# Kernel optimization log

Hardware: AMD Instinct MI355X
Metric: run time of the kernel (lower is better)

Reference implementation:

```python
import jax, jax.numpy as jnp
import numpy as np

D_MODEL = 1024
N_HEADS = 16
HEAD_DIM = D_MODEL // N_HEADS
MAX_LEN = 2048
BATCH = 2
SEQ = 2048


def setup_inputs() -> dict:
    key = jax.random.key(0)
    ks = jax.random.split(key, 6)
    std = 1.0 / np.sqrt(D_MODEL)
    x = jax.random.normal(ks[0], (BATCH, SEQ, D_MODEL), dtype=jnp.float32)
    Wqkv = jax.random.uniform(ks[1], (D_MODEL, 3 * D_MODEL), minval=-std, maxval=std, dtype=jnp.float32)
    bqkv = jax.random.uniform(ks[2], (3 * D_MODEL,), minval=-std, maxval=std, dtype=jnp.float32)
    Wout = jax.random.uniform(ks[3], (D_MODEL, D_MODEL), minval=-std, maxval=std, dtype=jnp.float32)
    bout = jax.random.uniform(ks[4], (D_MODEL,), minval=-std, maxval=std, dtype=jnp.float32)
    rel_pos_bias = 0.02 * jax.random.normal(ks[5], (2 * MAX_LEN - 1,), dtype=jnp.float32)
    return {"x": x, "Wqkv": Wqkv, "bqkv": bqkv, "Wout": Wout, "bout": bout, "rel_pos_bias": rel_pos_bias}


def reference(x, Wqkv, bqkv, Wout, bout, rel_pos_bias):
    B, S, _ = x.shape
    scale = HEAD_DIM ** -0.5
    qkv = x @ Wqkv + bqkv                       # [B,S,3*dm]
    qkv = qkv.reshape(B, S, 3, N_HEADS, HEAD_DIM)
    qkv = jnp.transpose(qkv, (2, 0, 3, 1, 4))   # [3,B,H,S,D]
    q, k, v = qkv[0], qkv[1], qkv[2]
    scores = jnp.einsum('bhqd,bhkd->bhqk', q, k) * scale
    pos = jnp.arange(S)
    rel = jnp.clip(pos[:, None] - pos[None, :] + (MAX_LEN - 1), 0, 2 * MAX_LEN - 2)
    scores = scores + rel_pos_bias[rel][None, None]  # bias shared over batch & heads
    probs = jax.nn.softmax(scores, axis=-1)
    out = jnp.einsum('bhqk,bhkd->bhqd', probs, v)    # [B,H,S,D]
    out = jnp.transpose(out, (0, 2, 1, 3)).reshape(B, S, D_MODEL)
    return out @ Wout + bout
```

## Files before the change

### kernel.cpp

```cpp
#include <hip/hip_runtime.h>
#include <cmath>

#define B_ 2
#define S_ 2048
#define H_ 16
#define D_ 64
#define DM 1024

typedef unsigned short u16;
using short8 = __attribute__((ext_vector_type(8))) short;
using f32x4  = __attribute__((ext_vector_type(4))) float;
using f32x16 = __attribute__((ext_vector_type(16))) float;
using i32x4  = __attribute__((ext_vector_type(4))) int;
typedef float uf4 __attribute__((ext_vector_type(4), aligned(4)));

__device__ __forceinline__ u16 f32_to_bf16(float f) {
    unsigned int u = __float_as_uint(f);
    u += 0x7fffu + ((u >> 16) & 1u);
    return (u16)(u >> 16);
}

__device__ __forceinline__ float exp2_fast(float x) {
    float r;
    asm("v_exp_f32 %0, %1" : "=v"(r) : "v"(x));
    return r;
}

__device__ __forceinline__ int cvt_pk_bf16(float lo, float hi) {
    int r;
    asm("v_cvt_pk_bf16_f32 %0, %1, %2" : "=v"(r) : "v"(lo), "v"(hi));
    return r;
}

__device__ __forceinline__ void gl_lds16(const void* src, void* dst) {
    __builtin_amdgcn_global_load_lds(
        (const __attribute__((address_space(1))) unsigned int*)src,
        (__attribute__((address_space(3))) unsigned int*)dst, 16, 0, 0);
}

__device__ __forceinline__ f32x16 mfma32(short8 a, short8 b, f32x16 c) {
    return __builtin_amdgcn_mfma_f32_32x32x16_bf16(a, b, c, 0, 0, 0);
}

__global__ __launch_bounds__(256) void relattn_prep(
    const float* __restrict__ x, const float* __restrict__ Wqkv,
    const float* __restrict__ Wout, const float* __restrict__ relb,
    u16* __restrict__ xb, u16* __restrict__ WqkvT, u16* __restrict__ WoutT,
    float* __restrict__ relb2)
{
    __shared__ float T[64][65];
    const int tid = threadIdx.x;
    int blk = blockIdx.x;
    if (blk >= 3072) {
        int i0 = ((blk - 3072) * 256 + tid) * 4;
#pragma unroll
        for (int j = 0; j < 4; ++j)
            if (i0 + j < 2 * 2048 - 1)
                relb2[i0 + j] = relb[i0 + j] * 1.44269504f;
        return;
    }
    if (blk < 2048) {
        size_t base = ((size_t)blk * 256 + tid) * 8;
        float4 v0 = *(const float4*)(x + base);
        float4 v1 = *(const float4*)(x + base + 4);
        ushort4 p0 = make_ushort4(f32_to_bf16(v0.x), f32_to_bf16(v0.y),
                                  f32_to_bf16(v0.z), f32_to_bf16(v0.w));
        ushort4 p1 = make_ushort4(f32_to_bf16(v1.x), f32_to_bf16(v1.y),
                                  f32_to_bf16(v1.z), f32_to_bf16(v1.w));
        *(ushort4*)(xb + base) = p0;
        *(ushort4*)(xb + base + 4) = p1;
        return;
    }
    int id = blk - 2048;
    const float* in; u16* outp; int R, C;
    if (id < 768) { in = Wqkv; outp = WqkvT; R = 1024; C = 3072; }
    else          { id -= 768; in = Wout;  outp = WoutT; R = 1024; C = 1024; }
    const int tpr = C >> 6;
    const int r0 = (id / tpr) << 6, c0 = (id % tpr) << 6;
#pragma unroll
    for (int it = 0; it < 4; ++it) {
        int e = tid + it * 256;
        int row = e >> 4, c4 = (e & 15) << 2;
        float4 v = *(const float4*)(in + (size_t)(r0 + row) * C + c0 + c4);
        T[row][c4 + 0] = v.x; T[row][c4 + 1] = v.y;
        T[row][c4 + 2] = v.z; T[row][c4 + 3] = v.w;
    }
    __syncthreads();
#pragma unroll
    for (int it = 0; it < 4; ++it) {
        int e = tid + it * 256;
        int crow = e >> 4, r4 = (e & 15) << 2;
        ushort4 pk = make_ushort4(f32_to_bf16(T[r4 + 0][crow]), f32_to_bf16(T[r4 + 1][crow]),
                                  f32_to_bf16(T[r4 + 2][crow]), f32_to_bf16(T[r4 + 3][crow]));
        *(ushort4*)(outp + (size_t)(c0 + crow) * R + r0 + r4) = pk;
    }
}

__global__ __launch_bounds__(256) void relattn_gemm_qkv(
    const u16* __restrict__ A, const u16* __restrict__ Bm,
    const float* __restrict__ bias, u16* __restrict__ qk, u16* __restrict__ Vt)
{
    __shared__ alignas(16) unsigned char AsB[16384];
    __shared__ alignas(16) unsigned char BsB[16384];
    const int tid = threadIdx.x;
    const int w = tid >> 6, l = tid & 63, ln = l & 15, hi = l >> 4;
    const int wr = w >> 1, wc = w & 1;
    const int row0 = blockIdx.y * 128, col0 = blockIdx.x * 128;
    const char* Ab = (const char*)A;
    const char* Bb = (const char*)Bm;

    f32x4 acc[4][4] = {};
    for (int step = 0; step < 16; ++step) {
        __syncthreads();
#pragma unroll
        for (int it = 0; it < 4; ++it) {
            int dsto = it * 4096 + w * 1024;
            int o = dsto + l * 16;
            int row = o >> 7;
            int swz = (o & 127) ^ ((row & 7) << 4);
            gl_lds16(Ab + (size_t)(row0 + row) * 2048 + step * 128 + swz, AsB + dsto);
            gl_lds16(Bb + (size_t)(col0 + row) * 2048 + step * 128 + swz, BsB + dsto);
        }
        __syncthreads();
#pragma unroll
        for (int kk = 0; kk < 2; ++kk) {
            short8 a[4], b[4];
            const int kb = hi * 16 + kk * 64;
#pragma unroll
            for (int m = 0; m < 4; ++m) {
                int row = wr * 64 + m * 16 + ln;
                a[m] = *(const short8*)(AsB + row * 128 + (kb ^ ((row & 7) << 4)));
            }
#pragma unroll
            for (int n = 0; n < 4; ++n) {
                int row = wc * 64 + n * 16 + ln;
                b[n] = *(const short8*)(BsB + row * 128 + (kb ^ ((row & 7) << 4)));
            }
#pragma unroll
            for (int m = 0; m < 4; ++m)
#pragma unroll
                for (int n = 0; n < 4; ++n)
                    acc[m][n] = __builtin_amdgcn_mfma_f32_16x16x32_bf16(a[m], b[n], acc[m][n], 0, 0, 0);
        }
    }

    const int t = col0 >> 10;
    const int bb = row0 >> 11;
    if (t < 2) {
#pragma unroll
        for (int n = 0; n < 4; ++n) {
            int c = col0 + wc * 64 + n * 16 + ln;
            int h = (c >> 6) & 15, d = c & 63;
            float bv = bias[c];
            u16* plane = qk + (size_t)((t * B_ + bb) * H_ + h) * S_ * D_;
#pragma unroll
            for (int m = 0; m < 4; ++m)
#pragma unroll
                for (int r = 0; r < 4; ++r) {
                    int s = (row0 + wr * 64 + m * 16 + hi * 4 + r) & (S_ - 1);
                    plane[(size_t)s * D_ + d] = f32_to_bf16(acc[m][n][r] + bv);
                }
        }
    } else {
#pragma unroll
        for (int n = 0; n < 4; ++n) {
            int c = col0 + wc * 64 + n * 16 + ln;
            int h = (c >> 6) & 15, d = c & 63;
            float bv = bias[c];
            u16* vrow = Vt + (size_t)((bb * H_ + h) * D_ + d) * S_;
#pragma unroll
            for (int m = 0; m < 4; ++m) {
                int s = (row0 + wr * 64 + m * 16 + hi * 4) & (S_ - 1);
                ushort4 pk = make_ushort4(f32_to_bf16(acc[m][n][0] + bv),
                                          f32_to_bf16(acc[m][n][1] + bv),
                                          f32_to_bf16(acc[m][n][2] + bv),
                                          f32_to_bf16(acc[m][n][3] + bv));
                *(ushort4*)(vrow + s) = pk;
            }
        }
    }
}

__global__ __launch_bounds__(512, 4) void relattn_attn(
    const u16* __restrict__ qk, const u16* __restrict__ Vt,
    const float* __restrict__ relb2, u16* __restrict__ aout)
{
    __shared__ alignas(16) unsigned char Lds[65536];
    const int tid = threadIdx.x;
    const int w = tid >> 6, l = tid & 63;
    const int wg = w & 3, g = w >> 2;
    const int l31 = l & 31, h2 = l >> 5;
    const int qt = blockIdx.x, bh = blockIdx.y;
    const int bb = bh >> 4;
    const char* qpl = (const char*)(qk + (size_t)bh * (S_ * D_));
    const char* kpl = (const char*)(qk + (size_t)(B_ * H_ + bh) * (S_ * D_));
    const char* vpl = (const char*)(Vt + (size_t)bh * (D_ * S_));
    unsigned char* GB = Lds + g * 32768;

    const int q0 = qt * 128 + wg * 32;
    const int qrow = q0 + l31;
    const int kvbase = g * 1024;

    short8 qf[4];
#pragma unroll
    for (int kd = 0; kd < 4; ++kd)
        qf[kd] = *(const short8*)(qpl + (size_t)qrow * 128 + kd * 32 + h2 * 16);

    f32x16 O0 = {}, O1 = {};
    float lrun = 0.f;

    {
#pragma unroll
        for (int it = 0; it < 2; ++it) {
            int dsto = it * 4096 + wg * 1024;
            int o = dsto + l * 16;
            int row = o >> 7;
            int swz = (o & 127) ^ ((row & 7) << 4);
            gl_lds16(kpl + (size_t)(kvbase + row) * 128 + swz, GB + dsto);
            gl_lds16(vpl + (size_t)row * (S_ * 2) + kvbase * 2 + swz, GB + 8192 + dsto);
        }
    }
    __syncthreads();

    for (int kt = 0; kt < 16; ++kt) {
        const int buf = kt & 1;
        const unsigned char* KB = GB + buf * 16384;
        const unsigned char* VB = KB + 8192;
        const int kv0 = kvbase + kt * 64;

        if (kt < 15) {
#pragma unroll
            for (int it = 0; it < 2; ++it) {
                int dsto = it * 4096 + wg * 1024;
                int o = dsto + l * 16;
                int row = o >> 7;
                int swz = (o & 127) ^ ((row & 7) << 4);
                unsigned char* db = GB + (buf ^ 1) * 16384 + dsto;
                gl_lds16(kpl + (size_t)(kv0 + 64 + row) * 128 + swz, db);
                gl_lds16(vpl + (size_t)row * (S_ * 2) + (kv0 + 64) * 2 + swz, db + 8192);
            }
        }

        const float* bp0 = relb2 + (qrow - kv0 - 4 * h2 + 2047);
        uf4 bv0[4], bv1[4];
#pragma unroll
        for (int rq = 0; rq < 4; ++rq) {
            bv0[rq] = *(const uf4*)(bp0 - 8 * rq - 3);
            bv1[rq] = *(const uf4*)(bp0 - 32 - 8 * rq - 3);
        }

        f32x16 s0 = {}, s1 = {};
#pragma unroll
        for (int kd = 0; kd < 4; ++kd) {
            int kbyte = kd * 32 + h2 * 16;
            int sw = (l31 & 7) << 4;
            short8 k0 = *(const short8*)(KB + l31 * 128 + (kbyte ^ sw));
            short8 k1 = *(const short8*)(KB + (32 + l31) * 128 + (kbyte ^ sw));
            s0 = mfma32(k0, qf[kd], s0);
            s1 = mfma32(k1, qf[kd], s1);
        }

        const float SC2 = 0.125f * 1.44269504f;
#pragma unroll
        for (int rq = 0; rq < 4; ++rq)
#pragma unroll
            for (int j = 0; j < 4; ++j) {
                s0[rq * 4 + j] = exp2_fast(s0[rq * 4 + j] * SC2 + bv0[rq][3 - j]);
                s1[rq * 4 + j] = exp2_fast(s1[rq * 4 + j] * SC2 + bv1[rq][3 - j]);
            }

        float q0s = ((s0[0] + s0[1]) + (s0[2] + s0[3])) + ((s0[4] + s0[5]) + (s0[6] + s0[7]));
        float q1s = ((s0[8] + s0[9]) + (s0[10] + s0[11])) + ((s0[12] + s0[13]) + (s0[14] + s0[15]));
        float q2s = ((s1[0] + s1[1]) + (s1[2] + s1[3])) + ((s1[4] + s1[5]) + (s1[6] + s1[7]));
        float q3s = ((s1[8] + s1[9]) + (s1[10] + s1[11])) + ((s1[12] + s1[13]) + (s1[14] + s1[15]));
        lrun += (q0s + q1s) + (q2s + q3s);

#pragma unroll
        for (int ts = 0; ts < 4; ++ts) {
            float p0, p1, p2, p3, p4, p5, p6, p7;
            if (ts == 0)      { p0=s0[0];  p1=s0[1];  p2=s0[2];  p3=s0[3];  p4=s0[4];  p5=s0[5];  p6=s0[6];  p7=s0[7]; }
            else if (ts == 1) { p0=s0[8];  p1=s0[9];  p2=s0[10]; p3=s0[11]; p4=s0[12]; p5=s0[13]; p6=s0[14]; p7=s0[15]; }
            else if (ts == 2) { p0=s1[0];  p1=s1[1];  p2=s1[2];  p3=s1[3];  p4=s1[4];  p5=s1[5];  p6=s1[6];  p7=s1[7]; }
            else              { p0=s1[8];  p1=s1[9];  p2=s1[10]; p3=s1[11]; p4=s1[12]; p5=s1[13]; p6=s1[14]; p7=s1[15]; }
            int c01 = cvt_pk_bf16(p0, p1), c23 = cvt_pk_bf16(p2, p3);
            int c45 = cvt_pk_bf16(p4, p5), c67 = cvt_pk_bf16(p6, p7);
            int px01 = __shfl_xor(c01, 32), px23 = __shfl_xor(c23, 32);
            int px45 = __shfl_xor(c45, 32), px67 = __shfl_xor(c67, 32);
            i32x4 pw;
            pw[0] = h2 ? px45 : c01;
            pw[1] = h2 ? px67 : c23;
            pw[2] = h2 ? c45 : px01;
            pw[3] = h2 ? c67 : px23;
            short8 pb = __builtin_bit_cast(short8, pw);
            int vbyte = ts * 32 + h2 * 16;
            int sw = (l31 & 7) << 4;
            short8 v0 = *(const short8*)(VB + l31 * 128 + (vbyte ^ sw));
            short8 v1 = *(const short8*)(VB + (32 + l31) * 128 + (vbyte ^ sw));
            O0 = mfma32(v0, pb, O0);
            O1 = mfma32(v1, pb, O1);
        }
        __syncthreads();
    }

    lrun += __shfl_xor(lrun, 32);

    {
        float* PO = (float*)(Lds + wg * 8448);
        float* PL = (float*)(Lds + wg * 8448 + 8192);
        if (g == 1) {
#pragma unroll
            for (int r = 0; r < 16; ++r) {
                PO[l * 32 + r] = O0[r];
                PO[l * 32 + 16 + r] = O1[r];
            }
            PL[l] = lrun;
        }
        __syncthreads();
        if (g == 1) return;
        float inv = 1.0f / (lrun + PL[l]);
        const float* src = PO + l * 32;
        u16* orow = aout + (size_t)(bb * S_ + qrow) * DM + (bh & 15) * 64 + 4 * h2;
#pragma unroll
        for (int gq = 0; gq < 4; ++gq) {
            float o00 = (O0[4*gq+0] + src[4*gq+0]) * inv;
            float o01 = (O0[4*gq+1] + src[4*gq+1]) * inv;
            float o02 = (O0[4*gq+2] + src[4*gq+2]) * inv;
            float o03 = (O0[4*gq+3] + src[4*gq+3]) * inv;
            float o10 = (O1[4*gq+0] + src[16+4*gq+0]) * inv;
            float o11 = (O1[4*gq+1] + src[16+4*gq+1]) * inv;
            float o12 = (O1[4*gq+2] + src[16+4*gq+2]) * inv;
            float o13 = (O1[4*gq+3] + src[16+4*gq+3]) * inv;
            ushort4 w0 = make_ushort4(f32_to_bf16(o00), f32_to_bf16(o01), f32_to_bf16(o02), f32_to_bf16(o03));
            ushort4 w1 = make_ushort4(f32_to_bf16(o10), f32_to_bf16(o11), f32_to_bf16(o12), f32_to_bf16(o13));
            *(ushort4*)(orow + 8 * gq) = w0;
            *(ushort4*)(orow + 32 + 8 * gq) = w1;
        }
    }
}

__global__ __launch_bounds__(256) void relattn_gemm_out(
    const u16* __restrict__ A, const u16* __restrict__ Bm,
    const float* __restrict__ bias, float* __restrict__ out)
{
    __shared__ alignas(16) unsigned char AsB[16384];
    __shared__ alignas(16) unsigned char BsB[16384];
    const int tid = threadIdx.x;
    const int w = tid >> 6, l = tid & 63, ln = l & 15, hi = l >> 4;
    const int wr = w >> 1, wc = w & 1;
    const int row0 = blockIdx.y * 128, col0 = blockIdx.x * 128;
    const char* Ab = (const char*)A;
    const char* Bb = (const char*)Bm;

    f32x4 acc[4][4] = {};
    for (int step = 0; step < 16; ++step) {
        __syncthreads();
#pragma unroll
        for (int it = 0; it < 4; ++it) {
            int dsto = it * 4096 + w * 1024;
            int o = dsto + l * 16;
            int row = o >> 7;
            int swz = (o & 127) ^ ((row & 7) << 4);
            gl_lds16(Ab + (size_t)(row0 + row) * 2048 + step * 128 + swz, AsB + dsto);
            gl_lds16(Bb + (size_t)(col0 + row) * 2048 + step * 128 + swz, BsB + dsto);
        }
        __syncthreads();
#pragma unroll
        for (int kk = 0; kk < 2; ++kk) {
            short8 a[4], b[4];
            const int kb = hi * 16 + kk * 64;
#pragma unroll
            for (int m = 0; m < 4; ++m) {
                int row = wr * 64 + m * 16 + ln;
                a[m] = *(const short8*)(AsB + row * 128 + (kb ^ ((row & 7) << 4)));
            }
#pragma unroll
            for (int n = 0; n < 4; ++n) {
                int row = wc * 64 + n * 16 + ln;
                b[n] = *(const short8*)(BsB + row * 128 + (kb ^ ((row & 7) << 4)));
            }
#pragma unroll
            for (int m = 0; m < 4; ++m)
#pragma unroll
                for (int n = 0; n < 4; ++n)
                    acc[m][n] = __builtin_amdgcn_mfma_f32_16x16x32_bf16(a[m], b[n], acc[m][n], 0, 0, 0);
        }
    }

#pragma unroll
    for (int n = 0; n < 4; ++n) {
        int c = col0 + wc * 64 + n * 16 + ln;
        float bv = bias[c];
#pragma unroll
        for (int m = 0; m < 4; ++m)
#pragma unroll
            for (int r = 0; r < 4; ++r) {
                int row = row0 + wr * 64 + m * 16 + hi * 4 + r;
                out[(size_t)row * DM + c] = acc[m][n][r] + bv;
            }
    }
}

extern "C" void kernel_launch(void* const* d_in, const int* in_sizes, int n_in,
                              void* d_out, int out_size, void* d_ws, size_t ws_size,
                              hipStream_t stream) {
    const float* x    = (const float*)d_in[0];
    const float* Wqkv = (const float*)d_in[1];
    const float* bqkv = (const float*)d_in[2];
    const float* Wout = (const float*)d_in[3];
    const float* bout = (const float*)d_in[4];
    const float* relb = (const float*)d_in[5];
    float* out = (float*)d_out;

    u16* ws    = (u16*)d_ws;
    u16* xb    = ws;
    u16* WqkvT = xb + 4194304;
    u16* WoutT = WqkvT + 3145728;
    u16* qkpl  = WoutT + 1048576;
    u16* Vt    = qkpl + 8388608;
    u16* aout  = Vt + 4194304;
    float* relb2 = (float*)(aout + 4194304);

    relattn_prep<<<3076, 256, 0, stream>>>(x, Wqkv, Wout, relb, xb, WqkvT, WoutT, relb2);
    relattn_gemm_qkv<<<dim3(24, 32), 256, 0, stream>>>(xb, WqkvT, bqkv, qkpl, Vt);
    relattn_attn<<<dim3(16, 32), 512, 0, stream>>>(qkpl, Vt, relb2, aout);
    relattn_gemm_out<<<dim3(8, 32), 256, 0, stream>>>(aout, WoutT, bout, out);
}
```

Before: 132.5 us.

## Drop intra-block KV split in attention; single group walks full key range

The attention kernel previously ran 512 threads per block as two groups of four waves, each covering half the key sequence, and merged their partial outputs through LDS at the end. Now each 256-thread block processes all 32 KV tiles with one group, which removes the cross-group reduction, its extra barrier and half the LDS. The cost is a longer serial loop per block and half as many waves per block, relying on higher block occupancy (launch bounds 256,5) to hide latency. The softmax here has no running-max rescaling, so the final normalization simply divides by the single running sum.

```diff
diff --git a/kernel.cpp b/kernel.cpp
--- a/kernel.cpp
+++ b/kernel.cpp
@@ -181,25 +181,21 @@
     }
 }
 
-__global__ __launch_bounds__(512, 4) void relattn_attn(
+__global__ __launch_bounds__(256, 5) void relattn_attn(
     const u16* __restrict__ qk, const u16* __restrict__ Vt,
     const float* __restrict__ relb2, u16* __restrict__ aout)
 {
-    __shared__ alignas(16) unsigned char Lds[65536];
+    __shared__ alignas(16) unsigned char Lds[32768];
     const int tid = threadIdx.x;
     const int w = tid >> 6, l = tid & 63;
-    const int wg = w & 3, g = w >> 2;
     const int l31 = l & 31, h2 = l >> 5;
     const int qt = blockIdx.x, bh = blockIdx.y;
     const int bb = bh >> 4;
     const char* qpl = (const char*)(qk + (size_t)bh * (S_ * D_));
     const char* kpl = (const char*)(qk + (size_t)(B_ * H_ + bh) * (S_ * D_));
     const char* vpl = (const char*)(Vt + (size_t)bh * (D_ * S_));
-    unsigned char* GB = Lds + g * 32768;
-
-    const int q0 = qt * 128 + wg * 32;
-    const int qrow = q0 + l31;
-    const int kvbase = g * 1024;
+
+    const int qrow = qt * 128 + w * 32 + l31;
 
     short8 qf[4];
 #pragma unroll
@@ -212,30 +208,30 @@
     {
 #pragma unroll
         for (int it = 0; it < 2; ++it) {
-            int dsto = it * 4096 + wg * 1024;
+            int dsto = it * 4096 + w * 1024;
             int o = dsto + l * 16;
             int row = o >> 7;
             int swz = (o & 127) ^ ((row & 7) << 4);
-            gl_lds16(kpl + (size_t)(kvbase + row) * 128 + swz, GB + dsto);
-            gl_lds16(vpl + (size_t)row * (S_ * 2) + kvbase * 2 + swz, GB + 8192 + dsto);
+            gl_lds16(kpl + (size_t)row * 128 + swz, Lds + dsto);
+            gl_lds16(vpl + (size_t)row * (S_ * 2) + swz, Lds + 8192 + dsto);
         }
     }
     __syncthreads();
 
-    for (int kt = 0; kt < 16; ++kt) {
+    for (int kt = 0; kt < 32; ++kt) {
         const int buf = kt & 1;
-        const unsigned char* KB = GB + buf * 16384;
+        const unsigned char* KB = Lds + buf * 16384;
         const unsigned char* VB = KB + 8192;
-        const int kv0 = kvbase + kt * 64;
-
-        if (kt < 15) {
+        const int kv0 = kt * 64;
+
+        if (kt < 31) {
 #pragma unroll
             for (int it = 0; it < 2; ++it) {
-                int dsto = it * 4096 + wg * 1024;
+                int dsto = it * 4096 + w * 1024;
                 int o = dsto + l * 16;
                 int row = o >> 7;
                 int swz = (o & 127) ^ ((row & 7) << 4);
-                unsigned char* db = GB + (buf ^ 1) * 16384 + dsto;
+                unsigned char* db = Lds + (buf ^ 1) * 16384 + dsto;
                 gl_lds16(kpl + (size_t)(kv0 + 64 + row) * 128 + swz, db);
                 gl_lds16(vpl + (size_t)row * (S_ * 2) + (kv0 + 64) * 2 + swz, db + 8192);
             }
@@ -303,38 +299,16 @@
     }
 
     lrun += __shfl_xor(lrun, 32);
-
-    {
-        float* PO = (float*)(Lds + wg * 8448);
-        float* PL = (float*)(Lds + wg * 8448 + 8192);
-        if (g == 1) {
-#pragma unroll
-            for (int r = 0; r < 16; ++r) {
-                PO[l * 32 + r] = O0[r];
-                PO[l * 32 + 16 + r] = O1[r];
-            }
-            PL[l] = lrun;
-        }
-        __syncthreads();
-        if (g == 1) return;
-        float inv = 1.0f / (lrun + PL[l]);
-        const float* src = PO + l * 32;
-        u16* orow = aout + (size_t)(bb * S_ + qrow) * DM + (bh & 15) * 64 + 4 * h2;
-#pragma unroll
-        for (int gq = 0; gq < 4; ++gq) {
-            float o00 = (O0[4*gq+0] + src[4*gq+0]) * inv;
-            float o01 = (O0[4*gq+1] + src[4*gq+1]) * inv;
-            float o02 = (O0[4*gq+2] + src[4*gq+2]) * inv;
-            float o03 = (O0[4*gq+3] + src[4*gq+3]) * inv;
-            float o10 = (O1[4*gq+0] + src[16+4*gq+0]) * inv;
-            float o11 = (O1[4*gq+1] + src[16+4*gq+1]) * inv;
-            float o12 = (O1[4*gq+2] + src[16+4*gq+2]) * inv;
-            float o13 = (O1[4*gq+3] + src[16+4*gq+3]) * inv;
-            ushort4 w0 = make_ushort4(f32_to_bf16(o00), f32_to_bf16(o01), f32_to_bf16(o02), f32_to_bf16(o03));
-            ushort4 w1 = make_ushort4(f32_to_bf16(o10), f32_to_bf16(o11), f32_to_bf16(o12), f32_to_bf16(o13));
-            *(ushort4*)(orow + 8 * gq) = w0;
-            *(ushort4*)(orow + 32 + 8 * gq) = w1;
-        }
+    float inv = 1.0f / lrun;
+    u16* orow = aout + (size_t)(bb * S_ + qrow) * DM + (bh & 15) * 64 + 4 * h2;
+#pragma unroll
+    for (int gq = 0; gq < 4; ++gq) {
+        ushort4 w0 = make_ushort4(f32_to_bf16(O0[4 * gq + 0] * inv), f32_to_bf16(O0[4 * gq + 1] * inv),
+                                  f32_to_bf16(O0[4 * gq + 2] * inv), f32_to_bf16(O0[4 * gq + 3] * inv));
+        ushort4 w1 = make_ushort4(f32_to_bf16(O1[4 * gq + 0] * inv), f32_to_bf16(O1[4 * gq + 1] * inv),
+                                  f32_to_bf16(O1[4 * gq + 2] * inv), f32_to_bf16(O1[4 * gq + 3] * inv));
+        *(ushort4*)(orow + 8 * gq) = w0;
+        *(ushort4*)(orow + 32 + 8 * gq) = w1;
     }
 }
 
@@ -422,6 +396,6 @@
 
     relattn_prep<<<3076, 256, 0, stream>>>(x, Wqkv, Wout, relb, xb, WqkvT, WoutT, relb2);
     relattn_gemm_qkv<<<dim3(24, 32), 256, 0, stream>>>(xb, WqkvT, bqkv, qkpl, Vt);
-    relattn_attn<<<dim3(16, 32), 512, 0, stream>>>(qkpl, Vt, relb2, aout);
+    relattn_attn<<<dim3(16, 32), 256, 0, stream>>>(qkpl, Vt, relb2, aout);
     relattn_gemm_out<<<dim3(8, 32), 256, 0, stream>>>(aout, WoutT, bout, out);
 }
```

Measured after the change: 206.7 us. 55.9% more time.
